# Performance work log

Hardware: AMD Instinct MI355X
Metric: run time of the kernel (lower is better)

## Reference

```python
import jax, jax.numpy as jnp
import numpy as np
from jax import lax

EMBED_DIM = 128
N_RELATIONS = 64
N_ENTITIES = 100000
N_EDGES = 600000


def setup_inputs() -> dict:
    key = jax.random.key(0)
    k1, k2, k3, k4, k5, k6 = jax.random.split(key, 6)
    entity_emb = jax.random.normal(k1, (N_ENTITIES, EMBED_DIM), dtype=jnp.float32)
    heads = jax.random.randint(k2, (N_EDGES,), 0, N_ENTITIES)
    rels = jax.random.randint(k3, (N_EDGES,), 0, N_RELATIONS)
    tails = jax.random.randint(k4, (N_EDGES,), 0, N_ENTITIES)
    # learned params: relation embedding table (std=0.01) and square Linear weight (xavier)
    rel_embed_weight = 0.01 * jax.random.normal(k5, (N_RELATIONS, EMBED_DIM), dtype=jnp.float32)
    xavier = float(np.sqrt(6.0 / (EMBED_DIM + EMBED_DIM)))
    W = jax.random.uniform(k6, (EMBED_DIM, EMBED_DIM), dtype=jnp.float32, minval=-xavier, maxval=xavier)
    return {"entity_emb": entity_emb, "rel_embed_weight": rel_embed_weight, "W": W,
            "heads": heads, "rels": rels, "tails": tails}


def reference(entity_emb, rel_embed_weight, W, heads, rels, tails):
    n_entities = entity_emb.shape[0]
    # gather edge endpoint / relation embeddings: [E, D]
    e_h = entity_emb[heads]
    e_t = entity_emb[tails]
    e_r = rel_embed_weight[rels]
    # tanh-gated dot-product score per edge: [E]
    score = jnp.sum(e_t * jnp.tanh(e_h + e_r), axis=-1)
    # global max-shift (detached in torch) then per-head segment softmax
    score_exp = jnp.exp(score - lax.stop_gradient(jnp.max(score)))
    score_sum = jax.ops.segment_sum(score_exp, heads, num_segments=n_entities)
    attn = score_exp / (score_sum[heads] + 1e-10)
    # scatter-add attention-weighted messages back to head nodes: [N, D]
    agg = jax.ops.segment_sum(attn[:, None] * e_t, heads, num_segments=n_entities)
    # final Linear (no bias) + LeakyReLU(0.2); dropout is identity in eval mode
    out = (entity_emb + agg) @ W.T
    return jax.nn.leaky_relu(out, negative_slope=0.2)
```

## Files before the change

### kernel.cpp

```cpp
#include <hip/hip_runtime.h>
#include <math.h>

#define EMBED 128
#define BMAX 8192
#define LDSPAD 136

#define TWO_LOG2E 2.8853900817779268f

typedef __attribute__((ext_vector_type(8))) short short8;
typedef __attribute__((ext_vector_type(4))) float floatx4;

__device__ __forceinline__ float ex2(float x) { return __builtin_amdgcn_exp2f(x); }

__device__ __forceinline__ float fast_tanh2(float x) {
    float e = ex2(TWO_LOG2E * x);
    return 1.0f - 2.0f * __builtin_amdgcn_rcpf(1.0f + e);
}

__device__ __forceinline__ unsigned short f2b(float f) {
    union { float f; unsigned int u; } v; v.f = f;
    unsigned int r = v.u + 0x7FFFu + ((v.u >> 16) & 1u);
    return (unsigned short)(r >> 16);
}

__device__ __forceinline__ float b2f(short u) {
    union { float f; unsigned int i; } v;
    v.i = ((unsigned int)(unsigned short)u) << 16;
    return v.f;
}

__global__ __launch_bounds__(256) void k_cast_hist(
    const float* __restrict__ ent, const float* __restrict__ rel, const float* __restrict__ W,
    short* __restrict__ entb, short* __restrict__ relb, short* __restrict__ wb,
    const int* __restrict__ heads, int* __restrict__ cnt,
    int ngE, int ngR, int ngW, int E)
{
    int stride = gridDim.x * 256;
    int total = ngE + ngR + ngW;
    for (int g = blockIdx.x * 256 + threadIdx.x; g < total; g += stride) {
        const float4* src; short* dst;
        if (g < ngE)            { src = (const float4*)ent + (size_t)g * 2;              dst = entb + (size_t)g * 8; }
        else if (g < ngE + ngR) { int g2 = g - ngE;       src = (const float4*)rel + (size_t)g2 * 2; dst = relb + (size_t)g2 * 8; }
        else                    { int g2 = g - ngE - ngR; src = (const float4*)W   + (size_t)g2 * 2; dst = wb   + (size_t)g2 * 8; }
        float4 a = src[0], b = src[1];
        short8 o;
        o[0] = (short)f2b(a.x); o[1] = (short)f2b(a.y); o[2] = (short)f2b(a.z); o[3] = (short)f2b(a.w);
        o[4] = (short)f2b(b.x); o[5] = (short)f2b(b.y); o[6] = (short)f2b(b.z); o[7] = (short)f2b(b.w);
        *(short8*)dst = o;
    }
    for (int e = blockIdx.x * 256 + threadIdx.x; e < E; e += stride)
        atomicAdd(cnt + heads[e], 1);
}

__global__ __launch_bounds__(1024) void k_scan1(
    const int* __restrict__ cnt, int* __restrict__ offs,
    int* __restrict__ bsum, int N)
{
    __shared__ int wsum[16];
    const int tid = threadIdx.x;
    int i = blockIdx.x * 1024 + tid;
    int v = (i < N) ? cnt[i] : 0;
    int x = v;
    #pragma unroll
    for (int d = 1; d < 64; d <<= 1) {
        int y = __shfl_up(x, d, 64);
        if ((tid & 63) >= d) x += y;
    }
    if ((tid & 63) == 63) wsum[tid >> 6] = x;
    __syncthreads();
    if (tid < 16) {
        int w = wsum[tid];
        #pragma unroll
        for (int d = 1; d < 16; d <<= 1) {
            int y = __shfl_up(w, d, 16);
            if (tid >= d) w += y;
        }
        wsum[tid] = w;
    }
    __syncthreads();
    int add = (tid >= 64) ? wsum[(tid >> 6) - 1] : 0;
    int incl = x + add;
    if (i < N) offs[i] = incl - v;
    if (tid == 1023) bsum[blockIdx.x] = incl;
}

__global__ __launch_bounds__(1024) void k_scan2(int* __restrict__ bsum, int nb)
{
    __shared__ int wsum[16];
    const int tid = threadIdx.x;
    int v = (tid < nb) ? bsum[tid] : 0;
    int x = v;
    #pragma unroll
    for (int d = 1; d < 64; d <<= 1) {
        int y = __shfl_up(x, d, 64);
        if ((tid & 63) >= d) x += y;
    }
    if ((tid & 63) == 63) wsum[tid >> 6] = x;
    __syncthreads();
    if (tid < 16) {
        int w = wsum[tid];
        #pragma unroll
        for (int d = 1; d < 16; d <<= 1) {
            int y = __shfl_up(w, d, 16);
            if (tid >= d) w += y;
        }
        wsum[tid] = w;
    }
    __syncthreads();
    int add = (tid >= 64) ? wsum[(tid >> 6) - 1] : 0;
    int incl = x + add;
    if (tid < nb) bsum[tid] = incl - v;
}

__global__ __launch_bounds__(256) void k_scan3(
    int* __restrict__ offs, const int* __restrict__ bsum,
    int* __restrict__ cursor, int N)
{
    int i = blockIdx.x * 256 + threadIdx.x;
    if (i < N) {
        int o = offs[i] + bsum[i >> 10];
        offs[i] = o;
        cursor[i] = o;
    }
}

__global__ __launch_bounds__(256) void k_csr(
    const int* __restrict__ heads, const int* __restrict__ rels,
    const int* __restrict__ tails, int* __restrict__ cursor,
    int2* __restrict__ tr, int E)
{
    int e = blockIdx.x * 256 + threadIdx.x;
    if (e >= E) return;
    int pos = atomicAdd(cursor + heads[e], 1);
    tr[pos] = make_int2(tails[e], rels[e]);
}

__global__ __launch_bounds__(256) void k_fused(
    const short* __restrict__ entb, const short* __restrict__ relb,
    const int* __restrict__ offs, const int* __restrict__ cnt,
    const int2* __restrict__ tr,
    short* __restrict__ accb, float* __restrict__ mh, float* __restrict__ lh,
    float* __restrict__ blockmax, int N, int R)
{
    __shared__ short rl[64 * EMBED];
    const int tid = threadIdx.x;
    if (R <= 64) {
        int nch = R * 16;
        for (int i = tid; i < nch; i += 256)
            ((short8*)rl)[i] = ((const short8*)relb)[i];
    }
    __syncthreads();
    const short* relsrc = (R <= 64) ? (const short*)rl : relb;

    const int lane = tid & 15;
    int head = blockIdx.x * 16 + (tid >> 4);
    float m = -INFINITY;
    if (head < N) {
        int start = offs[head];
        int c     = cnt[head];
        short8 hh = *((const short8*)(entb + (size_t)head * EMBED) + lane);
        float hf[8];
        #pragma unroll
        for (int i = 0; i < 8; ++i) hf[i] = b2f(hh[i]);
        float l = 0.f;
        float acc[8] = {0,0,0,0,0,0,0,0};
        for (int base = 0; base < c; base += 16) {
            int rem = c - base;
            int mm  = rem < 16 ? rem : 16;
            int2 trv = make_int2(0, 0);
            if (lane < mm) trv = tr[start + base + lane];
            for (int j = 0; j < mm; ++j) {
                int t = __shfl(trv.x, j, 16);
                int r = __shfl(trv.y, j, 16);
                short8 vt = *((const short8*)(entb + (size_t)t * EMBED) + lane);
                short8 vr = *((const short8*)(relsrc + (size_t)r * EMBED) + lane);
                float s = 0.f;
                #pragma unroll
                for (int i = 0; i < 8; ++i)
                    s += b2f(vt[i]) * fast_tanh2(hf[i] + b2f(vr[i]));
                s += __shfl_xor(s, 1, 16);
                s += __shfl_xor(s, 2, 16);
                s += __shfl_xor(s, 4, 16);
                s += __shfl_xor(s, 8, 16);
                float mn    = fmaxf(m, s);
                float alpha = __expf(m - mn);
                float p     = __expf(s - mn);
                l = l * alpha + p;
                #pragma unroll
                for (int q = 0; q < 8; ++q)
                    acc[q] = acc[q] * alpha + p * b2f(vt[q]);
                m = mn;
            }
        }
        short8 o;
        #pragma unroll
        for (int q = 0; q < 8; ++q) o[q] = (short)f2b(acc[q]);
        *((short8*)(accb + (size_t)head * EMBED) + lane) = o;
        if (lane == 0) { mh[head] = m; lh[head] = l; }
    }
    __shared__ float smax[256];
    smax[tid] = m;
    __syncthreads();
    for (int off = 128; off > 0; off >>= 1) {
        if (tid < off) smax[tid] = fmaxf(smax[tid], smax[tid + off]);
        __syncthreads();
    }
    if (tid == 0) blockmax[blockIdx.x] = smax[0];
}

__global__ __launch_bounds__(256) void k_maxred(
    const float* __restrict__ blockmax, float* __restrict__ Mout, int n)
{
    __shared__ float smax[256];
    float m = -INFINITY;
    for (int i = threadIdx.x; i < n; i += 256) m = fmaxf(m, blockmax[i]);
    smax[threadIdx.x] = m;
    __syncthreads();
    for (int off = 128; off > 0; off >>= 1) {
        if ((int)threadIdx.x < off)
            smax[threadIdx.x] = fmaxf(smax[threadIdx.x], smax[threadIdx.x + off]);
        __syncthreads();
    }
    if (threadIdx.x == 0) Mout[0] = smax[0];
}

__global__ __launch_bounds__(256) void k_gemm_f(
    const short* __restrict__ entb, const short* __restrict__ accb,
    const float* __restrict__ mh, const float* __restrict__ lh,
    const float* __restrict__ Mptr, const short* __restrict__ wb,
    float* __restrict__ out, int N)
{
    __shared__ short xs[128 * LDSPAD];
    __shared__ short ws[128 * LDSPAD];
    const int tid = threadIdx.x;
    const int n0  = blockIdx.x * 128;
    const float M = Mptr[0];

    #pragma unroll
    for (int it = 0; it < 8; ++it) {
        int ch = it * 256 + tid;
        int row = ch >> 4, col8 = ch & 15;
        *(short8*)(ws + row * LDSPAD + col8 * 8) = ((const short8*)wb)[ch];
    }
    #pragma unroll
    for (int it = 0; it < 8; ++it) {
        int ch = it * 256 + tid;
        int row = ch >> 4, col8 = ch & 15;
        int g = n0 + row;
        short8 v = {0,0,0,0,0,0,0,0};
        if (g < N) {
            float inv = 1.0f / (lh[g] + 1e-10f * __expf(M - mh[g]));
            short8 e8 = *((const short8*)(entb + (size_t)g * EMBED) + col8);
            short8 a8 = *((const short8*)(accb + (size_t)g * EMBED) + col8);
            #pragma unroll
            for (int q = 0; q < 8; ++q)
                v[q] = (short)f2b(b2f(e8[q]) + b2f(a8[q]) * inv);
        }
        *(short8*)(xs + row * LDSPAD + col8 * 8) = v;
    }
    __syncthreads();

    const int wv   = tid >> 6;
    const int lane = tid & 63;
    const int n16  = lane & 15;
    const int quad = lane >> 4;

    floatx4 acc[2][8];
    #pragma unroll
    for (int rt = 0; rt < 2; ++rt)
        #pragma unroll
        for (int jt = 0; jt < 8; ++jt)
            acc[rt][jt] = (floatx4){0.f, 0.f, 0.f, 0.f};

    #pragma unroll
    for (int kc = 0; kc < 4; ++kc) {
        int koff = kc * 32 + quad * 8;
        short8 a0 = *(const short8*)(xs + (wv * 32      + n16) * LDSPAD + koff);
        short8 a1 = *(const short8*)(xs + (wv * 32 + 16 + n16) * LDSPAD + koff);
        #pragma unroll
        for (int jt = 0; jt < 8; ++jt) {
            short8 b = *(const short8*)(ws + (jt * 16 + n16) * LDSPAD + koff);
            acc[0][jt] = __builtin_amdgcn_mfma_f32_16x16x32_bf16(a0, b, acc[0][jt], 0, 0, 0);
            acc[1][jt] = __builtin_amdgcn_mfma_f32_16x16x32_bf16(a1, b, acc[1][jt], 0, 0, 0);
        }
    }

    #pragma unroll
    for (int rt = 0; rt < 2; ++rt) {
        int rowbase = n0 + wv * 32 + rt * 16 + quad * 4;
        #pragma unroll
        for (int r = 0; r < 4; ++r) {
            int grow = rowbase + r;
            if (grow < N) {
                float* o = out + (size_t)grow * EMBED + n16;
                #pragma unroll
                for (int jt = 0; jt < 8; ++jt) {
                    float v = acc[rt][jt][r];
                    o[jt * 16] = (v > 0.f) ? v : 0.2f * v;
                }
            }
        }
    }
}

extern "C" void kernel_launch(void* const* d_in, const int* in_sizes, int n_in,
                              void* d_out, int out_size, void* d_ws, size_t ws_size,
                              hipStream_t stream)
{
    const float* ent   = (const float*)d_in[0];
    const float* rel   = (const float*)d_in[1];
    const float* W     = (const float*)d_in[2];
    const int*   heads = (const int*)d_in[3];
    const int*   rels  = (const int*)d_in[4];
    const int*   tails = (const int*)d_in[5];
    const int E = in_sizes[3];
    const int N = in_sizes[0] / EMBED;
    const int R = in_sizes[1] / EMBED;
    float* out = (float*)d_out;

    short* accb     = (short*)d_ws;
    float* mh       = (float*)(accb + (size_t)N * EMBED);
    float* lh       = mh + N;
    int2*  tr       = (int2*)(lh + N);
    int*   cnt      = (int*)(tr + E);
    int*   offs     = cnt + N;
    int*   cursor   = offs + N;
    float* blockmax = (float*)(cursor + N);
    float* Mval     = blockmax + BMAX;
    int*   bsum     = (int*)(Mval + 4);
    short* wb       = (short*)(bsum + 1024);
    short* entb     = wb + 16384;
    short* relb     = entb + (size_t)N * EMBED;

    const int nb  = (N + 1023) >> 10;
    const int ngh = (N + 15) / 16;

    hipMemsetAsync(cnt, 0, (size_t)N * sizeof(int), stream);

    int ngE = N * EMBED / 8, ngR = R * EMBED / 8, ngW = EMBED * EMBED / 8;
    k_cast_hist<<<2048, 256, 0, stream>>>(ent, rel, W, entb, relb, wb, heads, cnt, ngE, ngR, ngW, E);
    k_scan1<<<nb, 1024, 0, stream>>>(cnt, offs, bsum, N);
    k_scan2<<<1, 1024, 0, stream>>>(bsum, nb);
    k_scan3<<<(N + 255) / 256, 256, 0, stream>>>(offs, bsum, cursor, N);
    k_csr<<<(E + 255) / 256, 256, 0, stream>>>(heads, rels, tails, cursor, tr, E);
    k_fused<<<ngh, 256, 0, stream>>>(entb, relb, offs, cnt, tr, accb, mh, lh, blockmax, N, R);
    k_maxred<<<1, 256, 0, stream>>>(blockmax, Mval, ngh);
    k_gemm_f<<<(N + 127) / 128, 256, 0, stream>>>(entb, accb, mh, lh, Mval, wb, out, N);
}
```

Measured before the change: 252.3 us.

## Sort heads by degree to balance per-wavefront work in fused edge kernel

Builds a degree histogram during the scan, computes per-degree base offsets, and produces an order array that groups heads by in-degree via a counting sort. The fused attention kernel then processes heads in this order, so the 16-lane groups sharing a wavefront have equal edge counts. This is meant to reduce idle lanes from divergent loop trip counts. It adds atomics, an extra index indirection, and less spatial locality in head-indexed outputs.

```diff
diff --git a/kernel.cpp b/kernel.cpp
--- a/kernel.cpp
+++ b/kernel.cpp
@@ -4,6 +4,7 @@
 #define EMBED 128
 #define BMAX 8192
 #define LDSPAD 136
+#define DBINS 64
 
 #define TWO_LOG2E 2.8853900817779268f
 
@@ -32,9 +33,10 @@
 __global__ __launch_bounds__(256) void k_cast_hist(
     const float* __restrict__ ent, const float* __restrict__ rel, const float* __restrict__ W,
     short* __restrict__ entb, short* __restrict__ relb, short* __restrict__ wb,
-    const int* __restrict__ heads, int* __restrict__ cnt,
+    const int* __restrict__ heads, int* __restrict__ cnt, int* __restrict__ ghist,
     int ngE, int ngR, int ngW, int E)
 {
+    if (blockIdx.x == 0 && threadIdx.x < DBINS) ghist[threadIdx.x] = 0;
     int stride = gridDim.x * 256;
     int total = ngE + ngR + ngW;
     for (int g = blockIdx.x * 256 + threadIdx.x; g < total; g += stride) {
@@ -54,12 +56,16 @@
 
 __global__ __launch_bounds__(1024) void k_scan1(
     const int* __restrict__ cnt, int* __restrict__ offs,
-    int* __restrict__ bsum, int N)
+    int* __restrict__ bsum, int* __restrict__ ghist, int N)
 {
     __shared__ int wsum[16];
-    const int tid = threadIdx.x;
+    __shared__ int dh[DBINS];
+    const int tid = threadIdx.x;
+    if (tid < DBINS) dh[tid] = 0;
     int i = blockIdx.x * 1024 + tid;
     int v = (i < N) ? cnt[i] : 0;
+    __syncthreads();
+    if (i < N) atomicAdd(&dh[v < DBINS ? v : DBINS - 1], 1);
     int x = v;
     #pragma unroll
     for (int d = 1; d < 64; d <<= 1) {
@@ -82,9 +88,11 @@
     int incl = x + add;
     if (i < N) offs[i] = incl - v;
     if (tid == 1023) bsum[blockIdx.x] = incl;
-}
-
-__global__ __launch_bounds__(1024) void k_scan2(int* __restrict__ bsum, int nb)
+    if (tid < DBINS && dh[tid] > 0) atomicAdd(ghist + tid, dh[tid]);
+}
+
+__global__ __launch_bounds__(1024) void k_scan2(
+    int* __restrict__ bsum, int* __restrict__ ghist, int* __restrict__ dbase, int nb)
 {
     __shared__ int wsum[16];
     const int tid = threadIdx.x;
@@ -110,18 +118,45 @@
     int add = (tid >= 64) ? wsum[(tid >> 6) - 1] : 0;
     int incl = x + add;
     if (tid < nb) bsum[tid] = incl - v;
+    if (tid < DBINS) {
+        int g = ghist[tid];
+        int s = g;
+        #pragma unroll
+        for (int d = 1; d < 64; d <<= 1) {
+            int y = __shfl_up(s, d, 64);
+            if (tid >= d) s += y;
+        }
+        dbase[tid] = s - g;
+    }
 }
 
 __global__ __launch_bounds__(256) void k_scan3(
     int* __restrict__ offs, const int* __restrict__ bsum,
-    int* __restrict__ cursor, int N)
-{
-    int i = blockIdx.x * 256 + threadIdx.x;
+    int* __restrict__ cursor, const int* __restrict__ cnt,
+    int* __restrict__ dbase, int* __restrict__ order, int N)
+{
+    __shared__ int lcnt[DBINS];
+    __shared__ int lbase[DBINS];
+    const int tid = threadIdx.x;
+    if (tid < DBINS) lcnt[tid] = 0;
+    __syncthreads();
+    int i = blockIdx.x * 256 + tid;
+    int deg = 0, lrank = 0;
     if (i < N) {
         int o = offs[i] + bsum[i >> 10];
         offs[i] = o;
         cursor[i] = o;
-    }
+        int c = cnt[i];
+        deg = c < DBINS ? c : DBINS - 1;
+        lrank = atomicAdd(&lcnt[deg], 1);
+    }
+    __syncthreads();
+    if (tid < DBINS) {
+        int n = lcnt[tid];
+        lbase[tid] = n > 0 ? atomicAdd(dbase + tid, n) : 0;
+    }
+    __syncthreads();
+    if (i < N) order[lbase[deg] + lrank] = i;
 }
 
 __global__ __launch_bounds__(256) void k_csr(
@@ -138,7 +173,7 @@
 __global__ __launch_bounds__(256) void k_fused(
     const short* __restrict__ entb, const short* __restrict__ relb,
     const int* __restrict__ offs, const int* __restrict__ cnt,
-    const int2* __restrict__ tr,
+    const int2* __restrict__ tr, const int* __restrict__ order,
     short* __restrict__ accb, float* __restrict__ mh, float* __restrict__ lh,
     float* __restrict__ blockmax, int N, int R)
 {
@@ -153,7 +188,8 @@
     const short* relsrc = (R <= 64) ? (const short*)rl : relb;
 
     const int lane = tid & 15;
-    int head = blockIdx.x * 16 + (tid >> 4);
+    int head0 = blockIdx.x * 16 + (tid >> 4);
+    int head  = (head0 < N) ? order[head0] : N;
     float m = -INFINITY;
     if (head < N) {
         int start = offs[head];
@@ -328,7 +364,10 @@
     float* blockmax = (float*)(cursor + N);
     float* Mval     = blockmax + BMAX;
     int*   bsum     = (int*)(Mval + 4);
-    short* wb       = (short*)(bsum + 1024);
+    int*   ghist    = bsum + 1024;
+    int*   dbase    = ghist + DBINS;
+    int*   order    = dbase + DBINS;
+    short* wb       = (short*)(order + N);
     short* entb     = wb + 16384;
     short* relb     = entb + (size_t)N * EMBED;
 
@@ -338,12 +377,12 @@
     hipMemsetAsync(cnt, 0, (size_t)N * sizeof(int), stream);
 
     int ngE = N * EMBED / 8, ngR = R * EMBED / 8, ngW = EMBED * EMBED / 8;
-    k_cast_hist<<<2048, 256, 0, stream>>>(ent, rel, W, entb, relb, wb, heads, cnt, ngE, ngR, ngW, E);
-    k_scan1<<<nb, 1024, 0, stream>>>(cnt, offs, bsum, N);
-    k_scan2<<<1, 1024, 0, stream>>>(bsum, nb);
-    k_scan3<<<(N + 255) / 256, 256, 0, stream>>>(offs, bsum, cursor, N);
+    k_cast_hist<<<2048, 256, 0, stream>>>(ent, rel, W, entb, relb, wb, heads, cnt, ghist, ngE, ngR, ngW, E);
+    k_scan1<<<nb, 1024, 0, stream>>>(cnt, offs, bsum, ghist, N);
+    k_scan2<<<1, 1024, 0, stream>>>(bsum, ghist, dbase, nb);
+    k_scan3<<<(N + 255) / 256, 256, 0, stream>>>(offs, bsum, cursor, cnt, dbase, order, N);
     k_csr<<<(E + 255) / 256, 256, 0, stream>>>(heads, rels, tails, cursor, tr, E);
-    k_fused<<<ngh, 256, 0, stream>>>(entb, relb, offs, cnt, tr, accb, mh, lh, blockmax, N, R);
+    k_fused<<<ngh, 256, 0, stream>>>(entb, relb, offs, cnt, tr, order, accb, mh, lh, blockmax, N, R);
     k_maxred<<<1, 256, 0, stream>>>(blockmax, Mval, ngh);
     k_gemm_f<<<(N + 127) / 128, 256, 0, stream>>>(entb, accb, mh, lh, Mval, wb, out, N);
 }
```

Result: no change. 250.8 us (-0.6%).
